# Kernel optimization log

Measured on AMD Instinct MI355X. Metric: run time of the kernel, lower is better.

## Reference

```python
import jax, jax.numpy as jnp
import numpy as np

B, N, M, D, F, L = 128, 512, 512, 256, 512, 5
EPS = 1e-5  # torch InstanceNorm1d default eps


def setup_inputs() -> dict:
    key = jax.random.key(0)
    ks = jax.random.split(key, 12)
    s_d = 1.0 / np.sqrt(D)
    s_f = 1.0 / np.sqrt(F)
    return {
        "row_emb": jax.random.normal(ks[0], (B, N, D), jnp.float32),
        "col_emb": jax.random.normal(ks[1], (B, M, D), jnp.float32),
        "cost_mat": jax.random.uniform(ks[2], (B, N, M), jnp.float32),
        "log_scale": jnp.float32(np.log2(N)),
        "Wq": jax.random.normal(ks[3], (L, 2, D, D), jnp.float32) * s_d,
        "Wk": jax.random.normal(ks[4], (L, 2, D, D), jnp.float32) * s_d,
        "Wv": jax.random.normal(ks[5], (L, 2, D, D), jnp.float32) * s_d,
        "g1": jnp.ones((L, 2, D), jnp.float32),
        "be1": jnp.zeros((L, 2, D), jnp.float32),
        "W1": jax.random.normal(ks[6], (L, 2, D, F), jnp.float32) * s_d,
        "b1": jnp.zeros((L, 2, F), jnp.float32),
        "W2": jax.random.normal(ks[7], (L, 2, F, D), jnp.float32) * s_f,
        "b2": jnp.zeros((L, 2, D), jnp.float32),
        "g2": jnp.ones((L, 2, D), jnp.float32),
        "be2": jnp.zeros((L, 2, D), jnp.float32),
        "alpha": jnp.ones((L, 2), jnp.float32),
    }


def _instance_norm(x, g, b):
    # x: (B, seq, D); normalize over seq per (batch, channel), affine over D
    mu = x.mean(axis=1, keepdims=True)
    var = jnp.mean(jnp.square(x - mu), axis=1, keepdims=True)
    return (x - mu) * jax.lax.rsqrt(var + EPS) * g + b


def _aft(q, k, v, adaptation_bias):
    # Attention-free mixing: exp(bias) shared across numerator/denominator GEMMs
    E = jnp.exp(adaptation_bias)          # (B, n, m)
    ek = jnp.exp(k)                       # (B, m, D)
    num = jnp.einsum('bnm,bmd->bnd', E, ek * v)
    den = jnp.einsum('bnm,bmd->bnd', E, ek)
    weighted = jnp.nan_to_num(num / den)  # matches torch nan/inf safety net
    return jax.nn.sigmoid(q) * weighted


def _enc_block(xr, xc, cm, Wq, Wk, Wv, g1, be1, W1, b1, W2, b2, g2, be2, alpha):
    q = xr @ Wq
    k = xc @ Wk
    v = xc @ Wv
    out_aft = _aft(q, k, v, alpha * cm)
    h1 = _instance_norm(xr + out_aft, g1, be1)
    ff = jax.nn.relu(h1 @ W1 + b1) @ W2 + b2
    return _instance_norm(h1 + ff, g2, be2)


def reference(row_emb, col_emb, cost_mat, log_scale, Wq, Wk, Wv,
              g1, be1, W1, b1, W2, b2, g2, be2, alpha):
    cm = (-log_scale) * cost_mat          # (B, N, M)
    cmT = jnp.swapaxes(cm, 1, 2)          # (B, M, N)
    for l in range(L):
        new_row = _enc_block(row_emb, col_emb, cm,
                             Wq[l, 0], Wk[l, 0], Wv[l, 0], g1[l, 0], be1[l, 0],
                             W1[l, 0], b1[l, 0], W2[l, 0], b2[l, 0],
                             g2[l, 0], be2[l, 0], alpha[l, 0])
        new_col = _enc_block(col_emb, row_emb, cmT,
                             Wq[l, 1], Wk[l, 1], Wv[l, 1], g1[l, 1], be1[l, 1],
                             W1[l, 1], b1[l, 1], W2[l, 1], b2[l, 1],
                             g2[l, 1], be2[l, 1], alpha[l, 1])
        row_emb, col_emb = new_row, new_col
    return (row_emb, col_emb)
```

## Files before the change

### kernel.cpp

```cpp
#include <hip/hip_runtime.h>

typedef unsigned short u16;
typedef __attribute__((ext_vector_type(8))) short short8;
typedef __attribute__((ext_vector_type(4))) float f32x4;

#define DEVFUN __device__ __forceinline__

namespace {

constexpr int kB = 128;
constexpr int kN = 512;
constexpr int kD = 256;
constexpr int kF = 512;
constexpr int kL = 5;
constexpr float kEPS = 1e-5f;
constexpr long BND = (long)kB * kN * kD;

DEVFUN float bf2f(u16 u) {
  unsigned v = ((unsigned)u) << 16;
  float f;
  __builtin_memcpy(&f, &v, 4);
  return f;
}
DEVFUN u16 f2bf(float f) {
  unsigned x;
  __builtin_memcpy(&x, &f, 4);
  x = (x + 0x7FFFu + ((x >> 16) & 1u)) >> 16;
  return (u16)x;
}
DEVFUN u16 f2h(float f) {
  _Float16 h = (_Float16)f;
  u16 u;
  __builtin_memcpy(&u, &h, 2);
  return u;
}
DEVFUN float h2f(u16 u) {
  _Float16 h;
  __builtin_memcpy(&h, &u, 2);
  return (float)h;
}
DEVFUN float fsig(float x) { return 1.f / (1.f + __expf(-x)); }

union Pk8 { u16 p[8]; uint4 v; };
union Pk4 { u16 p[4]; uint2 v; };

DEVFUN void gload16(const u16* g, u16* l) {
  __builtin_amdgcn_global_load_lds(
      (const __attribute__((address_space(1))) void*)g,
      (__attribute__((address_space(3))) void*)l, 16, 0, 0);
}

DEVFUN void waitv8() { asm volatile("s_waitcnt vmcnt(8)" ::: "memory"); }
DEVFUN void waitv0() { asm volatile("s_waitcnt vmcnt(0)" ::: "memory"); }

template <int MODE>
__global__ __launch_bounds__(256) void tcvt(const float* __restrict__ src,
                                            u16* __restrict__ dst, int R,
                                            int C, const float* __restrict__ al,
                                            int pi, const float* __restrict__ ls) {
  __shared__ u16 T[64 * 64];
  const int t = threadIdx.x;
  const long z = blockIdx.z;
  const int cBase = blockIdx.x * 64, rBase = blockIdx.y * 64;
  float s = 0.f;
  if constexpr (MODE == 1) s = -al[pi] * ls[0];
#pragma unroll
  for (int i = 0; i < 4; ++i) {
    int u = i * 256 + t;
    int n = u >> 4, m4 = u & 15;
    float4 v = *(const float4*)(src + (z * R + rBase + n) * C + cBase + m4 * 4);
    Pk4 pk;
    if constexpr (MODE == 1) {
      pk.p[0] = f2bf(__expf(s * v.x)); pk.p[1] = f2bf(__expf(s * v.y));
      pk.p[2] = f2bf(__expf(s * v.z)); pk.p[3] = f2bf(__expf(s * v.w));
    } else if constexpr (MODE == 2) {
      pk.p[0] = f2h(v.x); pk.p[1] = f2h(v.y);
      pk.p[2] = f2h(v.z); pk.p[3] = f2h(v.w);
    } else {
      pk.p[0] = f2bf(v.x); pk.p[1] = f2bf(v.y);
      pk.p[2] = f2bf(v.z); pk.p[3] = f2bf(v.w);
    }
    int ch = (m4 >> 1) ^ ((n >> 3) & 7), hf = m4 & 1;
    *(uint2*)&T[n * 64 + ch * 8 + hf * 4] = pk.v;
  }
  __syncthreads();
#pragma unroll
  for (int j = 0; j < 2; ++j) {
    int u = j * 256 + t;
    int om = u >> 3, nc = u & 7;
    Pk8 pk;
#pragma unroll
    for (int i = 0; i < 8; ++i) {
      int n = nc * 8 + i;
      int ch = (om >> 3) ^ ((n >> 3) & 7);
      pk.p[i] = T[n * 64 + ch * 8 + (om & 7)];
    }
    *(uint4*)(dst + (z * C + cBase + om) * R + rBase + nc * 8) = pk.v;
  }
}

__global__ __launch_bounds__(256) void eexp(const float* __restrict__ src,
                                            u16* __restrict__ dst, long n8,
                                            const float* __restrict__ al,
                                            int pi, const float* __restrict__ ls) {
  const float s = -al[pi] * ls[0];
  for (long i = blockIdx.x * 256 + threadIdx.x; i < n8;
       i += (long)gridDim.x * 256) {
    const float* p = src + i * 8;
    float4 v0 = *(const float4*)p, v1 = *(const float4*)(p + 4);
    Pk8 pk;
    pk.p[0] = f2bf(__expf(s * v0.x)); pk.p[1] = f2bf(__expf(s * v0.y));
    pk.p[2] = f2bf(__expf(s * v0.z)); pk.p[3] = f2bf(__expf(s * v0.w));
    pk.p[4] = f2bf(__expf(s * v1.x)); pk.p[5] = f2bf(__expf(s * v1.y));
    pk.p[6] = f2bf(__expf(s * v1.z)); pk.p[7] = f2bf(__expf(s * v1.w));
    *(uint4*)(dst + i * 8) = pk.v;
  }
}

__global__ __launch_bounds__(256) void eexpH(const u16* __restrict__ src,
                                             u16* __restrict__ dst, long n8,
                                             const float* __restrict__ al,
                                             int pi, const float* __restrict__ ls) {
  const float s = -al[pi] * ls[0];
  for (long i = blockIdx.x * 256 + threadIdx.x; i < n8;
       i += (long)gridDim.x * 256) {
    Pk8 h;
    h.v = *(const uint4*)(src + i * 8);
    Pk8 pk;
#pragma unroll
    for (int q = 0; q < 8; ++q) pk.p[q] = f2bf(__expf(s * h2f(h.p[q])));
    *(uint4*)(dst + i * 8) = pk.v;
  }
}

template <int MODE>
__global__ __launch_bounds__(256) void cvtb(const float* __restrict__ src,
                                            u16* __restrict__ dst, long n8) {
  for (long i = blockIdx.x * 256 + threadIdx.x; i < n8;
       i += (long)gridDim.x * 256) {
    const float* p = src + i * 8;
    float4 v0 = *(const float4*)p, v1 = *(const float4*)(p + 4);
    Pk8 pk;
    if constexpr (MODE == 2) {
      pk.p[0] = f2h(v0.x); pk.p[1] = f2h(v0.y);
      pk.p[2] = f2h(v0.z); pk.p[3] = f2h(v0.w);
      pk.p[4] = f2h(v1.x); pk.p[5] = f2h(v1.y);
      pk.p[6] = f2h(v1.z); pk.p[7] = f2h(v1.w);
    } else {
      pk.p[0] = f2bf(v0.x); pk.p[1] = f2bf(v0.y);
      pk.p[2] = f2bf(v0.z); pk.p[3] = f2bf(v0.w);
      pk.p[4] = f2bf(v1.x); pk.p[5] = f2bf(v1.y);
      pk.p[6] = f2bf(v1.z); pk.p[7] = f2bf(v1.w);
    }
    *(uint4*)(dst + i * 8) = pk.v;
  }
}

DEVFUN void mfma_step(const u16* As, const u16* Bs, int wr, int wc, int lr,
                      int lhi, f32x4 acc[4][4]) {
#pragma unroll
  for (int ks = 0; ks < 2; ++ks) {
    short8 af[4], bfr[4];
#pragma unroll
    for (int m = 0; m < 4; ++m) {
      int r = wr + m * 16 + lr;
      af[m] = *(const short8*)&As[r * 64 + (((ks << 2) + lhi) ^ (r & 7)) * 8];
    }
#pragma unroll
    for (int n = 0; n < 4; ++n) {
      int r = wc + n * 16 + lr;
      bfr[n] = *(const short8*)&Bs[r * 64 + (((ks << 2) + lhi) ^ (r & 7)) * 8];
    }
#pragma unroll
    for (int m = 0; m < 4; ++m)
#pragma unroll
      for (int n = 0; n < 4; ++n)
        acc[m][n] = __builtin_amdgcn_mfma_f32_16x16x32_bf16(af[m], bfr[n],
                                                            acc[m][n], 0, 0, 0);
  }
}

enum Epi { EP_SIG = 0, EP_RELUB, EP_BIASRES };

template <int EPI, int KK>
__global__ __launch_bounds__(256) void gemm_mf(
    const u16* __restrict__ Asrc, const u16* __restrict__ WT, int gx,
    void* __restrict__ outp, const void* __restrict__ aux,
    const u16* __restrict__ aux2b, float* __restrict__ statsF) {
  __shared__ u16 SM[4 * 8192];
  const int t = threadIdx.x;
  const int lane = t & 63, wid = t >> 6;
  const int lr = lane & 15, lhi = lane >> 4;
  const int wr = (wid >> 1) * 64, wc = (wid & 1) * 64;
  const int cpx = gridDim.x >> 3;
  const int rb = (blockIdx.x & 7) * cpx + (blockIdx.x >> 3);
  const int bx = rb % gx;
  const long rowBase = (long)(rb / gx) * 128;
  const int colBase = bx * 128;
  const int r0 = wid * 32;
  const int rl = lane >> 3, sl = lane & 7;

  f32x4 acc[4][4];
#pragma unroll
  for (int m = 0; m < 4; ++m)
#pragma unroll
    for (int n = 0; n < 4; ++n) acc[m][n] = {0.f, 0.f, 0.f, 0.f};

  auto stage = [&](int tt, int pb) {
    const int kt = tt << 6;
    u16* As = SM + pb * 16384;
    u16* Bs = SM + pb * 16384 + 8192;
#pragma unroll
    for (int j = 0; j < 4; ++j) {
      int r = r0 + j * 8 + rl;
      int gch = sl ^ (r & 7);
      gload16(Asrc + (rowBase + r) * KK + kt + gch * 8, &As[(r0 + j * 8) * 64]);
      gload16(WT + (long)(colBase + r) * KK + kt + gch * 8,
              &Bs[(r0 + j * 8) * 64]);
    }
  };

  constexpr int NT = KK >> 6;
  stage(0, 0);
  stage(1, 1);
  waitv8();
  __builtin_amdgcn_s_barrier();
#pragma unroll
  for (int tt = 0; tt < NT - 1; ++tt) {
    mfma_step(SM + (tt & 1) * 16384, SM + (tt & 1) * 16384 + 8192, wr, wc, lr,
              lhi, acc);
    __builtin_amdgcn_s_barrier();
    if (tt + 2 < NT) {
      stage(tt + 2, tt & 1);
      waitv8();
    } else {
      waitv0();
    }
    __builtin_amdgcn_s_barrier();
  }
  mfma_step(SM + ((NT - 1) & 1) * 16384, SM + ((NT - 1) & 1) * 16384 + 8192,
            wr, wc, lr, lhi, acc);

  float psum[4] = {0.f, 0.f, 0.f, 0.f}, psq[4] = {0.f, 0.f, 0.f, 0.f};
#pragma unroll
  for (int m = 0; m < 4; ++m) {
#pragma unroll
    for (int n = 0; n < 4; ++n) {
#pragma unroll
      for (int rr = 0; rr < 4; ++rr) {
        float v = acc[m][n][rr];
        long grow = rowBase + wr + m * 16 + lhi * 4 + rr;
        int gcol = colBase + wc + n * 16 + lr;
        if constexpr (EPI == EP_SIG) {
          ((u16*)outp)[grow * 256 + gcol] = f2bf(fsig(v));
        } else if constexpr (EPI == EP_RELUB) {
          float bb = ((const float*)aux)[gcol];
          ((u16*)outp)[grow * 512 + gcol] = f2bf(fmaxf(v + bb, 0.f));
        } else {
          float bb = ((const float*)aux)[gcol];
          float y = v + bb + bf2f(aux2b[grow * 256 + gcol]);
          ((u16*)outp)[grow * 256 + gcol] = f2bf(y);
          psum[n] += y;
          psq[n] += y * y;
        }
      }
    }
  }

  if constexpr (EPI == EP_BIASRES) {
    __syncthreads();
    float* stS = (float*)SM;
    float* stQ = stS + 8 * 128;
    const int ctr = (wid >> 1) * 4 + lhi;
#pragma unroll
    for (int n = 0; n < 4; ++n) {
      stS[ctr * 128 + wc + n * 16 + lr] = psum[n];
      stQ[ctr * 128 + wc + n * 16 + lr] = psq[n];
    }
    __syncthreads();
    if (t < 128) {
      float s = 0.f, q = 0.f;
#pragma unroll
      for (int i = 0; i < 8; ++i) {
        s += stS[i * 128 + t];
        q += stQ[i * 128 + t];
      }
      const long b = rowBase >> 9;
      const int rblk = (int)((rowBase >> 7) & 3);
      const long o = ((b * 4 + rblk) * 256 + colBase + t) * 2;
      statsF[o] = s;
      statsF[o + 1] = q;
    }
  }
}

union KvSm {
  struct { u16 A[128 * 64]; u16 Bk[128 * 64]; u16 Bv[128 * 64]; } s;
  u16 T[128 * 128];
};

__global__ __launch_bounds__(256) void kv_mf(const u16* __restrict__ Asrc,
                                             const u16* __restrict__ WkT,
                                             const u16* __restrict__ WvT,
                                             u16* __restrict__ Cb) {
  __shared__ KvSm sm;
  const int t = threadIdx.x;
  const int lane = t & 63, wid = t >> 6;
  const int lr = lane & 15, lhi = lane >> 4;
  const int wr = (wid >> 1) * 64, wc = (wid & 1) * 64;
  const int cpx = gridDim.x >> 3;
  const int rb = (blockIdx.x & 7) * cpx + (blockIdx.x >> 3);
  const long rowBase = (long)(rb >> 1) * 128;
  const int colBase = (rb & 1) * 128;
  const long b = rowBase >> 9;
  const int mInB = (int)(rowBase & 511);
  const int r0 = wid * 32;
  const int rl = lane >> 3, sl = lane & 7;

  f32x4 ka[4][4], va[4][4];
#pragma unroll
  for (int m = 0; m < 4; ++m)
#pragma unroll
    for (int n = 0; n < 4; ++n) {
      ka[m][n] = {0.f, 0.f, 0.f, 0.f};
      va[m][n] = {0.f, 0.f, 0.f, 0.f};
    }

  for (int kt = 0; kt < 256; kt += 64) {
#pragma unroll
    for (int j = 0; j < 4; ++j) {
      int r = r0 + j * 8 + rl;
      int gch = sl ^ (r & 7);
      gload16(Asrc + (rowBase + r) * 256 + kt + gch * 8,
              &sm.s.A[(r0 + j * 8) * 64]);
      gload16(WkT + (long)(colBase + r) * 256 + kt + gch * 8,
              &sm.s.Bk[(r0 + j * 8) * 64]);
      gload16(WvT + (long)(colBase + r) * 256 + kt + gch * 8,
              &sm.s.Bv[(r0 + j * 8) * 64]);
    }
    __syncthreads();
    mfma_step(sm.s.A, sm.s.Bk, wr, wc, lr, lhi, ka);
    mfma_step(sm.s.A, sm.s.Bv, wr, wc, lr, lhi, va);
    __syncthreads();
  }

#pragma unroll
  for (int pass = 0; pass < 2; ++pass) {
#pragma unroll
    for (int m = 0; m < 4; ++m) {
#pragma unroll
      for (int n = 0; n < 4; ++n) {
        int m0 = wr + m * 16 + lhi * 4;
        int d = wc + n * 16 + lr;
        Pk4 pk;
#pragma unroll
        for (int rr = 0; rr < 4; ++rr) {
          float ek = __expf(ka[m][n][rr]);
          pk.p[rr] = f2bf(pass ? ek * va[m][n][rr] : ek);
        }
        int slot = (m0 >> 3) ^ (d & 7);
        *(uint2*)&sm.T[d * 128 + slot * 8 + (m0 & 7)] = pk.v;
      }
    }
    __syncthreads();
    const long rbase = b * 512 + (pass ? 0 : 256) + colBase;
#pragma unroll
    for (int j = 0; j < 8; ++j) {
      int idx = j * 256 + t;
      int d = idx >> 4, c = idx & 15;
      uint4 v = *(const uint4*)&sm.T[d * 128 + ((c ^ (d & 7)) * 8)];
      *(uint4*)(Cb + (rbase + d) * 512 + mInB + c * 8) = v;
    }
    __syncthreads();
  }
}

union SmU {
  struct { u16 A[128 * 64]; u16 B[128 * 64]; } s;
  struct { float den[128 * 68]; float st[2][8][64]; } d;
};

__global__ __launch_bounds__(256) void aft_mf(
    const u16* __restrict__ Ebuf, const u16* __restrict__ CbufT,
    const u16* __restrict__ qb, const u16* __restrict__ xrB,
    u16* __restrict__ dst, float* __restrict__ statsF) {
  __shared__ SmU sm;
  const int t = threadIdx.x;
  const int lane = t & 63, wid = t >> 6;
  const int lr = lane & 15, lhi = lane >> 4;
  const int wr = (wid >> 1) * 64, wc = (wid & 1) * 64;
  const int rb = (blockIdx.x & 7) * 256 + (blockIdx.x >> 3);
  const long b = rb >> 4;
  const int nBase = ((rb >> 2) & 3) * 128;
  const int dBase = (rb & 3) * 64;
  const int r0 = wid * 32;
  const int rl = lane >> 3, sl = lane & 7;

  f32x4 acc[4][4];
#pragma unroll
  for (int m = 0; m < 4; ++m)
#pragma unroll
    for (int n = 0; n < 4; ++n) acc[m][n] = {0.f, 0.f, 0.f, 0.f};

  for (int kt = 0; kt < 512; kt += 64) {
#pragma unroll
    for (int j = 0; j < 4; ++j) {
      int r = r0 + j * 8 + rl;
      int gch = sl ^ (r & 7);
      gload16(Ebuf + (b * 512 + nBase + r) * 512 + kt + gch * 8,
              &sm.s.A[(r0 + j * 8) * 64]);
      int gslot = (r < 64) ? (dBase + r) : (256 + dBase + (r - 64));
      gload16(CbufT + (b * 512 + gslot) * 512 + kt + gch * 8,
              &sm.s.B[(r0 + j * 8) * 64]);
    }
    __syncthreads();
    mfma_step(sm.s.A, sm.s.B, wr, wc, lr, lhi, acc);
    __syncthreads();
  }

  if (wc == 64) {
#pragma unroll
    for (int m = 0; m < 4; ++m)
#pragma unroll
      for (int n = 0; n < 4; ++n)
#pragma unroll
        for (int rr = 0; rr < 4; ++rr) {
          int nl = wr + m * 16 + lhi * 4 + rr;
          int dl = n * 16 + lr;
          sm.d.den[nl * 68 + dl] = acc[m][n][rr];
        }
  }
  __syncthreads();
  float psum[4] = {0.f, 0.f, 0.f, 0.f}, psq[4] = {0.f, 0.f, 0.f, 0.f};
  if (wc == 0) {
#pragma unroll
    for (int m = 0; m < 4; ++m)
#pragma unroll
      for (int n = 0; n < 4; ++n)
#pragma unroll
        for (int rr = 0; rr < 4; ++rr) {
          int nl = wr + m * 16 + lhi * 4 + rr;
          int dl = n * 16 + lr;
          float dv = sm.d.den[nl * 68 + dl];
          float w = acc[m][n][rr] / dv;
          if (!(w == w)) w = 0.f;
          else if (w > 3.402823466e38f) w = 3.402823466e38f;
          else if (w < -3.402823466e38f) w = -3.402823466e38f;
          long grow = b * 512 + nBase + nl;
          int gcol = dBase + dl;
          float sq = bf2f(qb[grow * 256 + gcol]);
          float y = bf2f(xrB[grow * 256 + gcol]) + sq * w;
          dst[grow * 256 + gcol] = f2bf(y);
          psum[n] += y;
          psq[n] += y * y;
        }
  }
  __syncthreads();
  if (wc == 0) {
    const int ctr = (wid >> 1) * 4 + lhi;
#pragma unroll
    for (int n = 0; n < 4; ++n) {
      sm.d.st[0][ctr][n * 16 + lr] = psum[n];
      sm.d.st[1][ctr][n * 16 + lr] = psq[n];
    }
  }
  __syncthreads();
  if (t < 64) {
    float s = 0.f, q = 0.f;
#pragma unroll
    for (int i = 0; i < 8; ++i) {
      s += sm.d.st[0][i][t];
      q += sm.d.st[1][i][t];
    }
    const long o = ((b * 4 + (nBase >> 7)) * 256 + dBase + t) * 2;
    statsF[o] = s;
    statsF[o + 1] = q;
  }
}

template <bool LASTF32>
__global__ __launch_bounds__(256) void inormS(const u16* __restrict__ Xin,
                                              const float* __restrict__ stats,
                                              const float* __restrict__ g,
                                              const float* __restrict__ be,
                                              u16* __restrict__ Xb,
                                              float* __restrict__ Xf) {
  const int b = blockIdx.x;
  const int ch0 = blockIdx.y * 64;
  const int t = threadIdx.x;
  const int lc = t & 63;
  const int ch = ch0 + lc;
  const int nr = t >> 6;
  const long base = (long)b * kN * kD + ch;

  __shared__ float s1[4][64], s2[4][64];
  __shared__ float mu[64], rs[64], gg[64], bb[64];
  {
    const long o = (((long)b * 4 + nr) * 256 + ch) * 2;
    s1[nr][lc] = stats[o];
    s2[nr][lc] = stats[o + 1];
  }
  __syncthreads();
  if (t < 64) {
    float ssum = s1[0][t] + s1[1][t] + s1[2][t] + s1[3][t];
    float ssq = s2[0][t] + s2[1][t] + s2[2][t] + s2[3][t];
    float m = ssum * (1.f / kN);
    float v = ssq * (1.f / kN) - m * m;
    mu[t] = m;
    rs[t] = rsqrtf(v + kEPS);
    gg[t] = g[ch0 + t];
    bb[t] = be[ch0 + t];
  }
  __syncthreads();
  const float m = mu[lc], rr = rs[lc], G = gg[lc], Bt = bb[lc];
  for (int n = nr; n < kN; n += 4) {
    long idx = base + (long)n * kD;
    float y = (bf2f(Xin[idx]) - m) * rr * G + Bt;
    Xb[idx] = f2bf(y);
    if constexpr (LASTF32) Xf[idx] = y;
  }
}

}

extern "C" void kernel_launch(void* const* d_in, const int* in_sizes, int n_in,
                              void* d_out, int out_size, void* d_ws,
                              size_t ws_size, hipStream_t stream) {
  (void)in_sizes; (void)n_in; (void)out_size;

  const float* in_row = (const float*)d_in[0];
  const float* in_col = (const float*)d_in[1];
  const float* cost = (const float*)d_in[2];
  const float* lsc = (const float*)d_in[3];
  const float* Wq = (const float*)d_in[4];
  const float* Wk = (const float*)d_in[5];
  const float* Wv = (const float*)d_in[6];
  const float* g1 = (const float*)d_in[7];
  const float* be1 = (const float*)d_in[8];
  const float* W1 = (const float*)d_in[9];
  const float* b1 = (const float*)d_in[10];
  const float* W2 = (const float*)d_in[11];
  const float* b2 = (const float*)d_in[12];
  const float* g2 = (const float*)d_in[13];
  const float* be2 = (const float*)d_in[14];
  const float* alpha = (const float*)d_in[15];

  float* outRow = (float*)d_out;
  float* outCol = outRow + BND;

  u16* qb = (u16*)d_ws;
  u16* h1b = qb;
  u16* CbufT = qb + BND;
  u16* ffmid = CbufT;
  u16* Ebuf = CbufT + 2 * BND;
  u16* bSt = Ebuf + 2 * BND;
  u16* h0b = bSt + 4 * BND;
  u16* h2b = h0b;
  u16* WqT = h0b + BND;
  u16* WkT = WqT + 10L * 256 * 256;
  u16* WvT = WkT + 10L * 256 * 256;
  u16* W1T = WvT + 10L * 256 * 256;
  u16* W2T = W1T + 10L * 512 * 256;
  float* statsF = (float*)(W2T + 10L * 256 * 512);
  u16* costTH = (u16*)(statsF + 128L * 4 * 256 * 2);
  u16* costH = costTH + 2 * BND;
  const long needElems = (long)(costH - (u16*)d_ws) + 2 * BND;
  const bool haveCH = (long)ws_size >= needElems * 2;

  const dim3 blk(256);
  tcvt<0><<<dim3(4, 4, 10), blk, 0, stream>>>(Wq, WqT, 256, 256, nullptr, 0, nullptr);
  tcvt<0><<<dim3(4, 4, 10), blk, 0, stream>>>(Wk, WkT, 256, 256, nullptr, 0, nullptr);
  tcvt<0><<<dim3(4, 4, 10), blk, 0, stream>>>(Wv, WvT, 256, 256, nullptr, 0, nullptr);
  tcvt<0><<<dim3(8, 4, 10), blk, 0, stream>>>(W1, W1T, 256, 512, nullptr, 0, nullptr);
  tcvt<0><<<dim3(4, 8, 10), blk, 0, stream>>>(W2, W2T, 512, 256, nullptr, 0, nullptr);
  cvtb<0><<<1024, blk, 0, stream>>>(in_row, bSt + 0 * BND, BND / 8);
  cvtb<0><<<1024, blk, 0, stream>>>(in_col, bSt + 1 * BND, BND / 8);
  if (haveCH) {
    tcvt<2><<<dim3(8, 8, 128), blk, 0, stream>>>(cost, costTH, 512, 512,
                                                 nullptr, 0, nullptr);
    cvtb<2><<<2048, blk, 0, stream>>>(cost, costH, 2 * BND / 8);
  }

  for (int l = 0; l < kL; ++l) {
    const int inPar = l & 1, outPar = 1 - inPar;
    const u16* bR = bSt + (inPar * 2 + 0) * BND;
    const u16* bC = bSt + (inPar * 2 + 1) * BND;

    for (int side = 0; side < 2; ++side) {
      const u16* xrB = side ? bC : bR;
      const u16* xcB = side ? bR : bC;
      u16* outB = bSt + (outPar * 2 + side) * BND;
      float* outF = side ? outCol : outRow;
      const int pi = l * 2 + side;

      if (side == 0) {
        if (haveCH)
          eexpH<<<4096, blk, 0, stream>>>(costH, Ebuf, 2 * BND / 8, alpha, pi,
                                          lsc);
        else
          eexp<<<4096, blk, 0, stream>>>(cost, Ebuf, 2 * BND / 8, alpha, pi,
                                         lsc);
      } else if (haveCH) {
        eexpH<<<4096, blk, 0, stream>>>(costTH, Ebuf, 2 * BND / 8, alpha, pi,
                                        lsc);
      } else {
        tcvt<1><<<dim3(8, 8, 128), blk, 0, stream>>>(cost, Ebuf, 512, 512,
                                                     alpha, pi, lsc);
      }

      gemm_mf<EP_SIG, 256><<<1024, blk, 0, stream>>>(
          xrB, WqT + (long)pi * 256 * 256, 2, qb, nullptr, nullptr, nullptr);
      kv_mf<<<1024, blk, 0, stream>>>(xcB, WkT + (long)pi * 256 * 256,
                                      WvT + (long)pi * 256 * 256, CbufT);
      aft_mf<<<2048, blk, 0, stream>>>(Ebuf, CbufT, qb, xrB, h0b, statsF);
      inormS<false><<<dim3(128, 4), blk, 0, stream>>>(
          h0b, statsF, g1 + pi * 256, be1 + pi * 256, h1b, nullptr);
      gemm_mf<EP_RELUB, 256><<<2048, blk, 0, stream>>>(
          h1b, W1T + (long)pi * 512 * 256, 4, ffmid, b1 + pi * 512, nullptr,
          nullptr);
      gemm_mf<EP_BIASRES, 512><<<1024, blk, 0, stream>>>(
          ffmid, W2T + (long)pi * 256 * 512, 2, h2b, b2 + pi * 256, h1b,
          statsF);
      if (l == kL - 1)
        inormS<true><<<dim3(128, 4), blk, 0, stream>>>(
            h2b, statsF, g2 + pi * 256, be2 + pi * 256, outB, outF);
      else
        inormS<false><<<dim3(128, 4), blk, 0, stream>>>(
            h2b, statsF, g2 + pi * 256, be2 + pi * 256, outB, nullptr);
    }
  }
}
```

Measured before the change: 3.299 ms.

## Fuse exp(bias) pass into kv kernel and single-buffer GEMM mainloop

Removes the standalone eexpH launch and appends its elementwise exp-of-scaled-cost work as a grid-stride tail inside kv_mf, cutting one kernel launch per side. It also replaces the double-buffered, async-prefetch GEMM mainloop with a single LDS buffer and load/sync/compute/sync per K tile. The single buffer halves LDS use, which may raise occupancy. The cost is that global loads no longer overlap MFMA work. The fused tail lengthens kv_mf and serializes the exp work behind the K/V projection.

```diff
diff --git a/kernel.cpp b/kernel.cpp
--- a/kernel.cpp
+++ b/kernel.cpp
@@ -49,9 +49,6 @@
       (const __attribute__((address_space(1))) void*)g,
       (__attribute__((address_space(3))) void*)l, 16, 0, 0);
 }
-
-DEVFUN void waitv8() { asm volatile("s_waitcnt vmcnt(8)" ::: "memory"); }
-DEVFUN void waitv0() { asm volatile("s_waitcnt vmcnt(0)" ::: "memory"); }
 
 template <int MODE>
 __global__ __launch_bounds__(256) void tcvt(const float* __restrict__ src,
@@ -113,22 +110,6 @@
     pk.p[2] = f2bf(__expf(s * v0.z)); pk.p[3] = f2bf(__expf(s * v0.w));
     pk.p[4] = f2bf(__expf(s * v1.x)); pk.p[5] = f2bf(__expf(s * v1.y));
     pk.p[6] = f2bf(__expf(s * v1.z)); pk.p[7] = f2bf(__expf(s * v1.w));
-    *(uint4*)(dst + i * 8) = pk.v;
-  }
-}
-
-__global__ __launch_bounds__(256) void eexpH(const u16* __restrict__ src,
-                                             u16* __restrict__ dst, long n8,
-                                             const float* __restrict__ al,
-                                             int pi, const float* __restrict__ ls) {
-  const float s = -al[pi] * ls[0];
-  for (long i = blockIdx.x * 256 + threadIdx.x; i < n8;
-       i += (long)gridDim.x * 256) {
-    Pk8 h;
-    h.v = *(const uint4*)(src + i * 8);
-    Pk8 pk;
-#pragma unroll
-    for (int q = 0; q < 8; ++q) pk.p[q] = f2bf(__expf(s * h2f(h.p[q])));
     *(uint4*)(dst + i * 8) = pk.v;
   }
 }
@@ -187,7 +168,9 @@
     const u16* __restrict__ Asrc, const u16* __restrict__ WT, int gx,
     void* __restrict__ outp, const void* __restrict__ aux,
     const u16* __restrict__ aux2b, float* __restrict__ statsF) {
-  __shared__ u16 SM[4 * 8192];
+  __shared__ u16 SM[2 * 8192];
+  u16* const As = SM;
+  u16* const Bs = SM + 8192;
   const int t = threadIdx.x;
   const int lane = t & 63, wid = t >> 6;
   const int lr = lane & 15, lhi = lane >> 4;
@@ -206,10 +189,7 @@
 #pragma unroll
     for (int n = 0; n < 4; ++n) acc[m][n] = {0.f, 0.f, 0.f, 0.f};
 
-  auto stage = [&](int tt, int pb) {
-    const int kt = tt << 6;
-    u16* As = SM + pb * 16384;
-    u16* Bs = SM + pb * 16384 + 8192;
+  for (int kt = 0; kt < KK; kt += 64) {
 #pragma unroll
     for (int j = 0; j < 4; ++j) {
       int r = r0 + j * 8 + rl;
@@ -218,28 +198,10 @@
       gload16(WT + (long)(colBase + r) * KK + kt + gch * 8,
               &Bs[(r0 + j * 8) * 64]);
     }
-  };
-
-  constexpr int NT = KK >> 6;
-  stage(0, 0);
-  stage(1, 1);
-  waitv8();
-  __builtin_amdgcn_s_barrier();
-#pragma unroll
-  for (int tt = 0; tt < NT - 1; ++tt) {
-    mfma_step(SM + (tt & 1) * 16384, SM + (tt & 1) * 16384 + 8192, wr, wc, lr,
-              lhi, acc);
-    __builtin_amdgcn_s_barrier();
-    if (tt + 2 < NT) {
-      stage(tt + 2, tt & 1);
-      waitv8();
-    } else {
-      waitv0();
-    }
-    __builtin_amdgcn_s_barrier();
-  }
-  mfma_step(SM + ((NT - 1) & 1) * 16384, SM + ((NT - 1) & 1) * 16384 + 8192,
-            wr, wc, lr, lhi, acc);
+    __syncthreads();
+    mfma_step(As, Bs, wr, wc, lr, lhi, acc);
+    __syncthreads();
+  }
 
   float psum[4] = {0.f, 0.f, 0.f, 0.f}, psq[4] = {0.f, 0.f, 0.f, 0.f};
 #pragma unroll
@@ -268,7 +230,6 @@
   }
 
   if constexpr (EPI == EP_BIASRES) {
-    __syncthreads();
     float* stS = (float*)SM;
     float* stQ = stS + 8 * 128;
     const int ctr = (wid >> 1) * 4 + lhi;
@@ -299,10 +260,11 @@
   u16 T[128 * 128];
 };
 
-__global__ __launch_bounds__(256) void kv_mf(const u16* __restrict__ Asrc,
-                                             const u16* __restrict__ WkT,
-                                             const u16* __restrict__ WvT,
-                                             u16* __restrict__ Cb) {
+__global__ __launch_bounds__(256) void kv_mf(
+    const u16* __restrict__ Asrc, const u16* __restrict__ WkT,
+    const u16* __restrict__ WvT, u16* __restrict__ Cb,
+    const u16* __restrict__ eSrcH, u16* __restrict__ Ebuf,
+    const float* __restrict__ al, int pi, const float* __restrict__ ls) {
   __shared__ KvSm sm;
   const int t = threadIdx.x;
   const int lane = t & 63, wid = t >> 6;
@@ -372,6 +334,20 @@
       *(uint4*)(Cb + (rbase + d) * 512 + mInB + c * 8) = v;
     }
     __syncthreads();
+  }
+
+  if (eSrcH != nullptr) {
+    const float s = -al[pi] * ls[0];
+    const long n8 = 2 * BND / 8;
+    const long stride = (long)gridDim.x * 256;
+    for (long i = (long)blockIdx.x * 256 + t; i < n8; i += stride) {
+      Pk8 h;
+      h.v = *(const uint4*)(eSrcH + i * 8);
+      Pk8 pk;
+#pragma unroll
+      for (int q = 0; q < 8; ++q) pk.p[q] = f2bf(__expf(s * h2f(h.p[q])));
+      *(uint4*)(Ebuf + i * 8) = pk.v;
+    }
   }
 }
 
@@ -593,16 +569,12 @@
       float* outF = side ? outCol : outRow;
       const int pi = l * 2 + side;
 
-      if (side == 0) {
-        if (haveCH)
-          eexpH<<<4096, blk, 0, stream>>>(costH, Ebuf, 2 * BND / 8, alpha, pi,
-                                          lsc);
-        else
-          eexp<<<4096, blk, 0, stream>>>(cost, Ebuf, 2 * BND / 8, alpha, pi,
-                                         lsc);
-      } else if (haveCH) {
-        eexpH<<<4096, blk, 0, stream>>>(costTH, Ebuf, 2 * BND / 8, alpha, pi,
-                                        lsc);
+      const u16* eH = nullptr;
+      if (haveCH) {
+        eH = side ? costTH : costH;
+      } else if (side == 0) {
+        eexp<<<4096, blk, 0, stream>>>(cost, Ebuf, 2 * BND / 8, alpha, pi,
+                                       lsc);
       } else {
         tcvt<1><<<dim3(8, 8, 128), blk, 0, stream>>>(cost, Ebuf, 512, 512,
                                                      alpha, pi, lsc);
@@ -611,7 +583,8 @@
       gemm_mf<EP_SIG, 256><<<1024, blk, 0, stream>>>(
           xrB, WqT + (long)pi * 256 * 256, 2, qb, nullptr, nullptr, nullptr);
       kv_mf<<<1024, blk, 0, stream>>>(xcB, WkT + (long)pi * 256 * 256,
-                                      WvT + (long)pi * 256 * 256, CbufT);
+                                      WvT + (long)pi * 256 * 256, CbufT, eH,
+                                      Ebuf, alpha, pi, lsc);
       aft_mf<<<2048, blk, 0, stream>>>(Ebuf, CbufT, qb, xrB, h0b, statsF);
       inormS<false><<<dim3(128, 4), blk, 0, stream>>>(
           h0b, statsF, g1 + pi * 256, be1 + pi * 256, h1b, nullptr);
```

After: 3.660 ms. 1.11x slower.
